# Kernel tuning notes

Measured on AMD Instinct MI355X. Metric: run time of the kernel, lower is better.

## Reference

```python
import jax, jax.numpy as jnp
import numpy as np

EPS = 1e-5  # GraphNorm eps


def setup_inputs() -> dict:
    key = jax.random.key(0)
    ks = jax.random.split(key, 8)
    B, N, D, L = 8, 2048, 128, 3
    return {
        "instance": jax.random.uniform(ks[0], (B, N, 2), jnp.float32),
        "Wn": jax.random.normal(ks[1], (D, 2), jnp.float32) * 0.5,
        "bn": jnp.zeros((D,), jnp.float32),
        "Wg": jax.random.normal(ks[2], (L, D, D), jnp.float32) / np.sqrt(D).astype(np.float32),
        "bg": jnp.zeros((L, D), jnp.float32),
        "gn_w": jnp.ones((D,), jnp.float32),
        "gn_b": jnp.zeros((D,), jnp.float32),
        "gn_a": jnp.ones((D,), jnp.float32),
    }


def reference(instance, Wn, bn, Wg, bg, gn_w, gn_b, gn_a):
    # instance: [B, N, 2] city coordinates. Graph is complete, so the PyG
    # edge-list GCN over all (i != j) pairs + self-loops is exactly a dense
    # symmetric-normalized adjacency matmul per graph.
    B, N, _ = instance.shape
    # pairwise Euclidean distances (cdist), safe sqrt to keep diagonal exact 0
    sq = jnp.sum(instance * instance, axis=-1)                      # [B, N]
    d2 = sq[:, :, None] + sq[:, None, :] - 2.0 * jnp.einsum(
        'bnd,bmd->bnm', instance, instance)                          # [B, N, N]
    pos = d2 > 0
    dist = jnp.where(pos, jnp.sqrt(jnp.where(pos, d2, 1.0)), 0.0)    # [B, N, N]
    # GCN edge weights = distances, self-loops added with weight 1.0
    A = dist + jnp.eye(N, dtype=dist.dtype)
    deg = jnp.sum(A, axis=-1)                                        # [B, N]
    dinv = jax.lax.rsqrt(deg)
    An = dinv[:, :, None] * A * dinv[:, None, :]                     # D^-1/2 A D^-1/2

    h = jnp.einsum('bne,de->bnd', instance, Wn) + bn                 # proj_node
    for l in range(Wg.shape[0]):
        # GCNConv: aggregate normalized messages of lin(x), then bias
        hw = jnp.einsum('bnm,bmd->bnd', An, jnp.einsum('bnd,ed->bne', h, Wg[l])) + bg[l]
        h = jnp.tanh(hw) + h                                         # activation + residual
        # GraphNorm (shared params across layers): per-graph, per-feature stats
        mean = jnp.mean(h, axis=1, keepdims=True)                    # [B, 1, D]
        sub = h - gn_a * mean
        var = jnp.mean(sub * sub, axis=1, keepdims=True)
        h = gn_w * sub * jax.lax.rsqrt(var + EPS) + gn_b
    return h  # [B, N, D] (unbatch+stack of equal-size graphs)
```

## Files before the change

kernel.cpp:

```cpp
#include <hip/hip_runtime.h>
#include <hip/hip_bf16.h>
#include <math.h>

#define BB 8
#define NN 2048
#define DD 128
#define LL 3
#define GN_EPS 1e-5f

typedef __attribute__((ext_vector_type(8))) short bf16x8;
typedef __attribute__((ext_vector_type(4))) float f32x4;
typedef __attribute__((ext_vector_type(8))) unsigned short u16x8;

#define FSQRT(x) __builtin_amdgcn_sqrtf(x)

__device__ __forceinline__ unsigned short f2bf(float f) {
    union { float f; unsigned u; } v; v.f = f;
    return (unsigned short)((v.u + 0x8000u) >> 16);
}

__device__ __forceinline__ float fast_tanh(float x) {
    float e = __expf(-2.0f * fabsf(x));
    float t = (1.0f - e) * __builtin_amdgcn_rcpf(1.0f + e);
    return copysignf(t, x);
}

__device__ __forceinline__ void stats_sc(float ps, float pq, float a, float w_,
                                         float b_, float& s, float& c) {
    const float inv_n = 1.0f / (float)NN;
    float mean = ps * inv_n;
    float msq  = pq * inv_n;
    float var  = msq - mean * mean * a * (2.0f - a);
    float rstd = rsqrtf(var + GN_EPS);
    s = w_ * rstd;
    c = b_ - s * (a * mean);
}


__global__ __launch_bounds__(256)
void prep_wg(const float* __restrict__ Wg, const float* __restrict__ Wn,
             const float* __restrict__ bn, unsigned short* __restrict__ wgf,
             float* __restrict__ weff, float* __restrict__ beff)
{
    const int f = blockIdx.x * 256 + threadIdx.x;
    const int l  = f >> 14;
    const int r  = f & 16383;
    const int dp = r >> 7;
    const int e  = r & 127;
    const int dpt = dp >> 4, ll = dp & 15;
    const int kc  = e >> 5,  eo = e & 31;
    wgf[((((l * 8 + dpt) * 4 + kc) * 16 + ll) << 5) + eo] = f2bf(Wg[f]);

    if (blockIdx.x == 0 && threadIdx.x < 128) {
        const int ee = threadIdx.x;
        float a0 = 0.f, a1 = 0.f, cc = 0.f;
        for (int d = 0; d < 128; ++d) {
            const float wv = Wg[ee * 128 + d];
            a0 = fmaf(wv, Wn[d * 2 + 0], a0);
            a1 = fmaf(wv, Wn[d * 2 + 1], a1);
            cc = fmaf(wv, bn[d], cc);
        }
        weff[ee * 2 + 0] = a0;
        weff[ee * 2 + 1] = a1;
        beff[ee] = cc;
    }
}

__global__ __launch_bounds__(256)
void gen_pack(const float* __restrict__ inst, const float* __restrict__ Wn,
              const float* __restrict__ bn, const float* __restrict__ weff,
              const float* __restrict__ beff,
              float* __restrict__ dinv, float* __restrict__ h,
              unsigned short* __restrict__ tp,
              float* __restrict__ psum, float* __restrict__ psq)
{
    __shared__ float cs[NN * 2];
    __shared__ float part[4][16];
    const int b     = blockIdx.x & 7;
    const int ntile = blockIdx.x >> 3;
    const int n0    = ntile * 16;
    const int tid   = threadIdx.x;
    const int w     = tid >> 6;
    const int lane  = tid & 63;
    const int lq    = lane >> 4;
    const int ll    = lane & 15;

    const float* instb = inst + b * NN * 2;
    for (int i = tid; i < (NN * 2) / 4; i += 256)
        ((float4*)cs)[i] = ((const float4*)instb)[i];
    __syncthreads();

    const int n = n0 + ll;
    const float nx = cs[n * 2 + 0];
    const float ny = cs[n * 2 + 1];

    const int diagkcg = ntile >> 1;
    float rs = 0.f;
    for (int kc = 0; kc < 16; ++kc) {
        const int kcg = w * 16 + kc;
        const int mb  = kcg * 32 + lq * 8;
        const float* cp = &cs[mb * 2];
        float4 c01 = *(const float4*)(cp + 0);
        float4 c23 = *(const float4*)(cp + 4);
        float4 c45 = *(const float4*)(cp + 8);
        float4 c67 = *(const float4*)(cp + 12);
        float mxx[8] = { c01.x, c01.z, c23.x, c23.z, c45.x, c45.z, c67.x, c67.z };
        float myy[8] = { c01.y, c01.w, c23.y, c23.w, c45.y, c45.w, c67.y, c67.w };
        float dist[8];
        #pragma unroll
        for (int j = 0; j < 8; ++j) {
            float dx = nx - mxx[j];
            float dy = ny - myy[j];
            dist[j] = FSQRT(dx * dx + dy * dy);
        }
        if (kcg == diagkcg) {
            #pragma unroll
            for (int j = 0; j < 8; ++j)
                if (mb + j == n) dist[j] = 1.0f;
        }
        #pragma unroll
        for (int j = 0; j < 8; ++j) rs += dist[j];
    }

    rs += __shfl_xor(rs, 16);
    rs += __shfl_xor(rs, 32);
    if (lq == 0) part[w][ll] = rs;
    __syncthreads();
    if (tid < 16)
        dinv[b * NN + n0 + tid] = rsqrtf(part[0][tid] + part[1][tid] +
                                         part[2][tid] + part[3][tid]);

    {
        const int d  = tid & 127;
        const int r0 = tid >> 7;
        const float w0 = Wn[d * 2 + 0];
        const float w1 = Wn[d * 2 + 1];
        const float bv = bn[d];
        const float we0 = weff[d * 2 + 0];
        const float we1 = weff[d * 2 + 1];
        const float be  = beff[d];
        const int kcg   = ntile >> 1;
        const int mbase = (ntile & 1) * 16;
        const int dt    = d >> 4;
        const int lld   = d & 15;
        unsigned short* tpd =
            tp + (((size_t)(b * 64 + kcg) * 8 + dt) * 64 + lld) * 8;
        #pragma unroll
        for (int r = r0; r < 16; r += 2) {
            const float x0 = cs[(n0 + r) * 2 + 0];
            const float x1 = cs[(n0 + r) * 2 + 1];
            h[((size_t)b * NN + n0 + r) * DD + d] = fmaf(x0, w0, fmaf(x1, w1, bv));
            const float dv = rsqrtf(part[0][r] + part[1][r] + part[2][r] + part[3][r]);
            const int mloc = mbase + r;
            const int lqa  = mloc >> 3;
            const int j    = mloc & 7;
            tpd[(size_t)lqa * 128 + j] = f2bf(dv * fmaf(x0, we0, fmaf(x1, we1, be)));
        }
    }
    if (blockIdx.x == 0) {
        for (int i = tid; i < LL * BB * DD; i += 256) { psum[i] = 0.f; psq[i] = 0.f; }
    }
}

template <bool HP>
__global__ __launch_bounds__(256)
void lin_mfma(const float* __restrict__ h, const unsigned short* __restrict__ wgf_l,
              const float* __restrict__ dinv,
              const float* __restrict__ psumP, const float* __restrict__ psqP,
              const float* __restrict__ ga, const float* __restrict__ gw,
              const float* __restrict__ gb, unsigned short* __restrict__ tp)
{
    __shared__ float sL[DD], cL[DD];
    const int tid  = threadIdx.x;
    const int b    = blockIdx.x & 7;
    const int tile = blockIdx.x >> 3;
    const int row0 = b * NN + tile * 32;
    const int w    = tid >> 6;
    const int lane = tid & 63;
    const int lq   = lane >> 4;
    const int ll   = lane & 15;

    if (tid < DD) {
        float s = 1.0f, c = 0.0f;
        if (HP)
            stats_sc(psumP[b * DD + tid], psqP[b * DD + tid],
                     ga[tid], gw[tid], gb[tid], s, c);
        sL[tid] = s; cL[tid] = c;
    }
    __syncthreads();

    bf16x8 aw[2][4];
    #pragma unroll
    for (int mt = 0; mt < 2; ++mt) {
        const int dpt = 2 * w + mt;
        #pragma unroll
        for (int kc = 0; kc < 4; ++kc)
            aw[mt][kc] = *(const bf16x8*)&wgf_l[(((dpt * 4 + kc) * 16 + ll) << 5) + lq * 8];
    }

    bf16x8 bh[2][4];
    #pragma unroll
    for (int nt = 0; nt < 2; ++nt) {
        const float* hrow = h + (size_t)(row0 + nt * 16 + ll) * DD;
        #pragma unroll
        for (int kc = 0; kc < 4; ++kc) {
            float4 h0 = *(const float4*)&hrow[kc * 32 + lq * 8];
            float4 h1 = *(const float4*)&hrow[kc * 32 + lq * 8 + 4];
            const int e0 = kc * 32 + lq * 8;
            bf16x8 p;
            p[0] = (short)f2bf(fmaf(sL[e0 + 0], h0.x, cL[e0 + 0]));
            p[1] = (short)f2bf(fmaf(sL[e0 + 1], h0.y, cL[e0 + 1]));
            p[2] = (short)f2bf(fmaf(sL[e0 + 2], h0.z, cL[e0 + 2]));
            p[3] = (short)f2bf(fmaf(sL[e0 + 3], h0.w, cL[e0 + 3]));
            p[4] = (short)f2bf(fmaf(sL[e0 + 4], h1.x, cL[e0 + 4]));
            p[5] = (short)f2bf(fmaf(sL[e0 + 5], h1.y, cL[e0 + 5]));
            p[6] = (short)f2bf(fmaf(sL[e0 + 6], h1.z, cL[e0 + 6]));
            p[7] = (short)f2bf(fmaf(sL[e0 + 7], h1.w, cL[e0 + 7]));
            bh[nt][kc] = p;
        }
    }

    f32x4 acc[2][2];
    #pragma unroll
    for (int i = 0; i < 2; ++i)
        #pragma unroll
        for (int j = 0; j < 2; ++j) acc[i][j] = (f32x4)0.0f;

    #pragma unroll
    for (int kc = 0; kc < 4; ++kc)
        #pragma unroll
        for (int nt = 0; nt < 2; ++nt)
            #pragma unroll
            for (int mt = 0; mt < 2; ++mt)
                acc[nt][mt] = __builtin_amdgcn_mfma_f32_16x16x32_bf16(
                    bh[nt][kc], aw[mt][kc], acc[nt][mt], 0, 0, 0);

    #pragma unroll
    for (int nt = 0; nt < 2; ++nt) {
        const int mloc0 = nt * 16 + lq * 4;
        const int lq_a  = mloc0 >> 3;
        const int j0    = mloc0 & 7;
        float4 di4 = *(const float4*)&dinv[row0 + mloc0];
        #pragma unroll
        for (int mt = 0; mt < 2; ++mt) {
            const int dt = 2 * w + mt;
            ushort4 pk;
            pk.x = f2bf(acc[nt][mt][0] * di4.x);
            pk.y = f2bf(acc[nt][mt][1] * di4.y);
            pk.z = f2bf(acc[nt][mt][2] * di4.z);
            pk.w = f2bf(acc[nt][mt][3] * di4.w);
            *(ushort4*)&tp[((size_t)((b * 64 + tile) * 8 + dt) * 64 + lq_a * 16 + ll) * 8 + j0] = pk;
        }
    }
}

template <bool HP>
__global__ __launch_bounds__(256, 2)
void agg_mfma(const float* __restrict__ inst, const unsigned short* __restrict__ tp,
              const float* __restrict__ dinv, const float* __restrict__ bg_l,
              const float* __restrict__ psumP, const float* __restrict__ psqP,
              const float* __restrict__ ga, const float* __restrict__ gw,
              const float* __restrict__ gb,
              float* __restrict__ h, float* __restrict__ psum, float* __restrict__ psq)
{
    __shared__ float cs[NN * 2];
    __shared__ char Abuf[64 * 1024];
    const int b    = blockIdx.x & 7;
    const int t2   = blockIdx.x >> 3;
    const int n0   = t2 * 32;
    const int tid  = threadIdx.x;
    const int w    = tid >> 6;
    const int lane = tid & 63;
    const int lq   = lane >> 4;
    const int ll   = lane & 15;

    const float* instb = inst + b * NN * 2;
    for (int i = tid; i < (NN * 2) / 4; i += 256)
        ((float4*)cs)[i] = ((const float4*)instb)[i];

    const unsigned short* tpb = tp + ((size_t)b * 64 * 8) * 512 + lane * 8;

    f32x4 acc[2][2];
    acc[0][0] = (f32x4)0.0f; acc[0][1] = (f32x4)0.0f;
    acc[1][0] = (f32x4)0.0f; acc[1][1] = (f32x4)0.0f;

    bf16x8 fbA0[4], fbA1[4], fbB0[4], fbB1[4];

    __syncthreads();

    const int   nr0 = n0 + ll;
    const int   nr1 = n0 + 16 + ll;
    const float nx0 = cs[nr0 * 2 + 0], ny0 = cs[nr0 * 2 + 1];
    const float nx1 = cs[nr1 * 2 + 0], ny1 = cs[nr1 * 2 + 1];

#define LOADB_INTO(B0, B1, KK) { \
        _Pragma("unroll") \
        for (int s_ = 0; s_ < 4; ++s_) { \
            B0[s_] = *(const bf16x8*)(tpb + (size_t)(((KK) * 4 + s_) * 8 + 2 * w + 0) * 512); \
            B1[s_] = *(const bf16x8*)(tpb + (size_t)(((KK) * 4 + s_) * 8 + 2 * w + 1) * 512); \
        } \
    }

#define GENPH(PH) { \
        _Pragma("unroll") \
        for (int q = 0; q < 8; ++q) { \
            const int kcg = (PH) * 32 + w * 8 + q; \
            const int mb  = kcg * 32 + lq * 8; \
            const float* cp = &cs[mb * 2]; \
            float4 c01 = *(const float4*)(cp + 0); \
            float4 c23 = *(const float4*)(cp + 4); \
            float4 c45 = *(const float4*)(cp + 8); \
            float4 c67 = *(const float4*)(cp + 12); \
            float mxx[8] = { c01.x, c01.z, c23.x, c23.z, c45.x, c45.z, c67.x, c67.z }; \
            float myy[8] = { c01.y, c01.w, c23.y, c23.w, c45.y, c45.w, c67.y, c67.w }; \
            const int slot0 = (2 * w + (q >> 2)) * 8 + (q & 3); \
            const bool dk = (kcg == t2); \
            u16x8 pk0, pk1; \
            _Pragma("unroll") \
            for (int j = 0; j < 8; ++j) { \
                float dx0 = nx0 - mxx[j], dy0 = ny0 - myy[j]; \
                float dv0 = FSQRT(dx0 * dx0 + dy0 * dy0); \
                if (dk && mb + j == nr0) dv0 = 1.0f; \
                pk0[j] = f2bf(dv0); \
                float dx1 = nx1 - mxx[j], dy1 = ny1 - myy[j]; \
                float dv1 = FSQRT(dx1 * dx1 + dy1 * dy1); \
                if (dk && mb + j == nr1) dv1 = 1.0f; \
                pk1[j] = f2bf(dv1); \
            } \
            *(u16x8*)(Abuf + (slot0 + 0) * 1024 + lane * 16) = pk0; \
            *(u16x8*)(Abuf + (slot0 + 4) * 1024 + lane * 16) = pk1; \
        } \
    }

#define STEP(I, C0, C1, DOLOAD, N0, N1, KN) { \
        bf16x8 af[2][4]; \
        _Pragma("unroll") \
        for (int nt = 0; nt < 2; ++nt) \
            _Pragma("unroll") \
            for (int s = 0; s < 4; ++s) \
                af[nt][s] = *(const bf16x8*)(Abuf + (((I) * 8 + nt * 4 + s) * 1024) + lane * 16); \
        if (DOLOAD) LOADB_INTO(N0, N1, KN) \
        _Pragma("unroll") \
        for (int s = 0; s < 4; ++s) \
            _Pragma("unroll") \
            for (int nt = 0; nt < 2; ++nt) { \
                acc[nt][0] = __builtin_amdgcn_mfma_f32_16x16x32_bf16(C0[s], af[nt][s], acc[nt][0], 0, 0, 0); \
                acc[nt][1] = __builtin_amdgcn_mfma_f32_16x16x32_bf16(C1[s], af[nt][s], acc[nt][1], 0, 0, 0); \
            } \
    }

    LOADB_INTO(fbA0, fbA1, 0)

    GENPH(0)
    __syncthreads();
    STEP(0, fbA0, fbA1, true,  fbB0, fbB1, 1)
    STEP(1, fbB0, fbB1, true,  fbA0, fbA1, 2)
    STEP(2, fbA0, fbA1, true,  fbB0, fbB1, 3)
    STEP(3, fbB0, fbB1, true,  fbA0, fbA1, 4)
    STEP(4, fbA0, fbA1, true,  fbB0, fbB1, 5)
    STEP(5, fbB0, fbB1, true,  fbA0, fbA1, 6)
    STEP(6, fbA0, fbA1, true,  fbB0, fbB1, 7)
    STEP(7, fbB0, fbB1, true,  fbA0, fbA1, 8)
    __syncthreads();

    GENPH(1)
    __syncthreads();
    STEP(0, fbA0, fbA1, true,  fbB0, fbB1, 9)
    STEP(1, fbB0, fbB1, true,  fbA0, fbA1, 10)
    STEP(2, fbA0, fbA1, true,  fbB0, fbB1, 11)
    STEP(3, fbB0, fbB1, true,  fbA0, fbA1, 12)
    STEP(4, fbA0, fbA1, true,  fbB0, fbB1, 13)
    STEP(5, fbB0, fbB1, true,  fbA0, fbA1, 14)
    STEP(6, fbA0, fbA1, true,  fbB0, fbB1, 15)
    STEP(7, fbB0, fbB1, false, fbA0, fbA1, 0)
    __syncthreads();

#undef STEP
#undef GENPH
#undef LOADB_INTO

    const float di0 = dinv[b * NN + n0 + ll];
    const float di1 = dinv[b * NN + n0 + 16 + ll];
    #pragma unroll
    for (int dtl = 0; dtl < 2; ++dtl) {
        const int d0 = (2 * w + dtl) * 16 + lq * 4;
        float4 bg4 = *(const float4*)&bg_l[d0];
        float sres[4] = {1.f, 1.f, 1.f, 1.f}, cres[4] = {0.f, 0.f, 0.f, 0.f};
        if (HP) {
            float4 ps4 = *(const float4*)&psumP[b * DD + d0];
            float4 pq4 = *(const float4*)&psqP[b * DD + d0];
            float4 ga4 = *(const float4*)&ga[d0];
            float4 gw4 = *(const float4*)&gw[d0];
            float4 gb4 = *(const float4*)&gb[d0];
            stats_sc(ps4.x, pq4.x, ga4.x, gw4.x, gb4.x, sres[0], cres[0]);
            stats_sc(ps4.y, pq4.y, ga4.y, gw4.y, gb4.y, sres[1], cres[1]);
            stats_sc(ps4.z, pq4.z, ga4.z, gw4.z, gb4.z, sres[2], cres[2]);
            stats_sc(ps4.w, pq4.w, ga4.w, gw4.w, gb4.w, sres[3], cres[3]);
        }
        float hs[4] = {0.f, 0.f, 0.f, 0.f}, hq[4] = {0.f, 0.f, 0.f, 0.f};
        #pragma unroll
        for (int nt = 0; nt < 2; ++nt) {
            const int n = n0 + nt * 16 + ll;
            const float di = nt ? di1 : di0;
            size_t idx = ((size_t)b * NN + n) * DD + d0;
            float4 hv = *(const float4*)&h[idx];
            float outv[4];
            #pragma unroll
            for (int r = 0; r < 4; ++r) {
                float pre = di * acc[nt][dtl][r] + (&bg4.x)[r];
                outv[r] = fast_tanh(pre) + fmaf(sres[r], (&hv.x)[r], cres[r]);
                hs[r] += outv[r];
                hq[r] += outv[r] * outv[r];
            }
            float4 ov = { outv[0], outv[1], outv[2], outv[3] };
            *(float4*)&h[idx] = ov;
        }

        #pragma unroll
        for (int off = 1; off < 16; off <<= 1) {
            #pragma unroll
            for (int r = 0; r < 4; ++r) {
                hs[r] += __shfl_xor(hs[r], off);
                hq[r] += __shfl_xor(hq[r], off);
            }
        }
        if (ll == 0) {
            #pragma unroll
            for (int r = 0; r < 4; ++r) {
                atomicAdd(&psum[b * DD + d0 + r], hs[r]);
                atomicAdd(&psq[b * DD + d0 + r], hq[r]);
            }
        }
    }
}

__global__ __launch_bounds__(256)
void apply_kernel(const float* __restrict__ h,
                  const float* __restrict__ psum2, const float* __restrict__ psq2,
                  const float* __restrict__ ga, const float* __restrict__ gw,
                  const float* __restrict__ gb, float* __restrict__ dst)
{
    const int i4 = blockIdx.x * 256 + threadIdx.x;
    const int dg = (i4 & 31) * 4;
    const int b  = i4 >> 16;
    float4 hv = ((const float4*)h)[i4];
    float o[4];
    #pragma unroll
    for (int j = 0; j < 4; ++j) {
        const int d = dg + j;
        float s, c;
        stats_sc(psum2[b * DD + d], psq2[b * DD + d], ga[d], gw[d], gb[d], s, c);
        o[j] = fmaf(s, (&hv.x)[j], c);
    }
    float4 ov = { o[0], o[1], o[2], o[3] };
    ((float4*)dst)[i4] = ov;
}

extern "C" void kernel_launch(void* const* d_in, const int* in_sizes, int n_in,
                              void* d_out, int out_size, void* d_ws, size_t ws_size,
                              hipStream_t stream)
{
    const float* inst = (const float*)d_in[0];
    const float* Wn   = (const float*)d_in[1];
    const float* bn   = (const float*)d_in[2];
    const float* Wg   = (const float*)d_in[3];
    const float* bg   = (const float*)d_in[4];
    const float* gw   = (const float*)d_in[5];
    const float* gb   = (const float*)d_in[6];
    const float* ga   = (const float*)d_in[7];
    float* out = (float*)d_out;

    float* ws   = (float*)d_ws;
    float* dinv = ws;
    float* h    = dinv + BB * NN;
    float* psum = h + (size_t)BB * NN * DD;
    float* psq  = psum + LL * BB * DD;
    float* weff = psq + LL * BB * DD;
    float* beff = weff + 2 * DD;
    unsigned short* wgf = (unsigned short*)(beff + DD);
    unsigned short* tp  = wgf + LL * DD * DD;

    prep_wg<<<(LL * DD * DD) / 256, 256, 0, stream>>>(Wg, Wn, bn, wgf, weff, beff);
    gen_pack<<<1024, 256, 0, stream>>>(inst, Wn, bn, weff, beff, dinv, h, tp, psum, psq);

    agg_mfma<false><<<512, 256, 0, stream>>>(
        inst, tp, dinv, bg + 0 * DD, nullptr, nullptr, ga, gw, gb, h, psum, psq);

    for (int l = 1; l < LL; ++l) {
        const unsigned short* wgl = wgf + (size_t)l * DD * DD;
        const float* psP = psum + (size_t)(l - 1) * BB * DD;
        const float* pqP = psq  + (size_t)(l - 1) * BB * DD;
        float* psL = psum + (size_t)l * BB * DD;
        float* pqL = psq  + (size_t)l * BB * DD;
        lin_mfma<true><<<(BB * NN) / 32, 256, 0, stream>>>(
            h, wgl, dinv, psP, pqP, ga, gw, gb, tp);
        agg_mfma<true><<<512, 256, 0, stream>>>(
            inst, tp, dinv, bg + l * DD, psP, pqP, ga, gw, gb, h, psL, pqL);
    }
    apply_kernel<<<(BB * NN * DD / 4) / 256, 256, 0, stream>>>(
        h, psum + 2 * BB * DD, psq + 2 * BB * DD, ga, gw, gb, out);
}
```

Baseline: 198.9 us.

## Double-buffer distance tiles in LDS and interleave generation with MFMA steps

Splits the 64KB adjacency staging buffer into two 32KB planes and generates the next quarter of on-the-fly distance tiles while MFMAs consume the current plane. Each wave now interleaves sqrt/bf16 packing with matrix instructions, so ALU and matrix work can overlap instead of running in separate phases. The number of block barriers grows, and register pressure goes up because generation temporaries are live alongside the B-fragment double buffers. The diagonal self-loop fix is hoisted under a per-tile branch.

```diff
diff --git a/kernel.cpp b/kernel.cpp
--- a/kernel.cpp
+++ b/kernel.cpp
@@ -264,7 +264,7 @@
               float* __restrict__ h, float* __restrict__ psum, float* __restrict__ psq)
 {
     __shared__ float cs[NN * 2];
-    __shared__ char Abuf[64 * 1024];
+    __shared__ __align__(16) char plane[2][32768];
     const int b    = blockIdx.x & 7;
     const int t2   = blockIdx.x >> 3;
     const int n0   = t2 * 32;
@@ -301,44 +301,45 @@
         } \
     }
 
-#define GENPH(PH) { \
+#define GENQ(PL, PH, Q) { \
+        const int kcg_ = (PH) * 16 + w * 4 + (Q); \
+        const int mb_  = kcg_ * 32 + lq * 8; \
+        const float* cp_ = &cs[mb_ * 2]; \
+        float4 c01 = *(const float4*)(cp_ + 0); \
+        float4 c23 = *(const float4*)(cp_ + 4); \
+        float4 c45 = *(const float4*)(cp_ + 8); \
+        float4 c67 = *(const float4*)(cp_ + 12); \
+        float mxx[8] = { c01.x, c01.z, c23.x, c23.z, c45.x, c45.z, c67.x, c67.z }; \
+        float myy[8] = { c01.y, c01.w, c23.y, c23.w, c45.y, c45.w, c67.y, c67.w }; \
+        float dv0[8], dv1[8]; \
         _Pragma("unroll") \
-        for (int q = 0; q < 8; ++q) { \
-            const int kcg = (PH) * 32 + w * 8 + q; \
-            const int mb  = kcg * 32 + lq * 8; \
-            const float* cp = &cs[mb * 2]; \
-            float4 c01 = *(const float4*)(cp + 0); \
-            float4 c23 = *(const float4*)(cp + 4); \
-            float4 c45 = *(const float4*)(cp + 8); \
-            float4 c67 = *(const float4*)(cp + 12); \
-            float mxx[8] = { c01.x, c01.z, c23.x, c23.z, c45.x, c45.z, c67.x, c67.z }; \
-            float myy[8] = { c01.y, c01.w, c23.y, c23.w, c45.y, c45.w, c67.y, c67.w }; \
-            const int slot0 = (2 * w + (q >> 2)) * 8 + (q & 3); \
-            const bool dk = (kcg == t2); \
-            u16x8 pk0, pk1; \
+        for (int j = 0; j < 8; ++j) { \
+            float dx0 = nx0 - mxx[j], dy0 = ny0 - myy[j]; \
+            dv0[j] = FSQRT(dx0 * dx0 + dy0 * dy0); \
+            float dx1 = nx1 - mxx[j], dy1 = ny1 - myy[j]; \
+            dv1[j] = FSQRT(dx1 * dx1 + dy1 * dy1); \
+        } \
+        if (kcg_ == t2) {    \
             _Pragma("unroll") \
             for (int j = 0; j < 8; ++j) { \
-                float dx0 = nx0 - mxx[j], dy0 = ny0 - myy[j]; \
-                float dv0 = FSQRT(dx0 * dx0 + dy0 * dy0); \
-                if (dk && mb + j == nr0) dv0 = 1.0f; \
-                pk0[j] = f2bf(dv0); \
-                float dx1 = nx1 - mxx[j], dy1 = ny1 - myy[j]; \
-                float dv1 = FSQRT(dx1 * dx1 + dy1 * dy1); \
-                if (dk && mb + j == nr1) dv1 = 1.0f; \
-                pk1[j] = f2bf(dv1); \
+                if (mb_ + j == nr0) dv0[j] = 1.0f; \
+                if (mb_ + j == nr1) dv1[j] = 1.0f; \
             } \
-            *(u16x8*)(Abuf + (slot0 + 0) * 1024 + lane * 16) = pk0; \
-            *(u16x8*)(Abuf + (slot0 + 4) * 1024 + lane * 16) = pk1; \
         } \
-    }
-
-#define STEP(I, C0, C1, DOLOAD, N0, N1, KN) { \
+        u16x8 pk0, pk1; \
+        _Pragma("unroll") \
+        for (int j = 0; j < 8; ++j) { pk0[j] = f2bf(dv0[j]); pk1[j] = f2bf(dv1[j]); } \
+        *(u16x8*)(plane[PL] + (w * 8 + 0 + (Q)) * 1024 + lane * 16) = pk0; \
+        *(u16x8*)(plane[PL] + (w * 8 + 4 + (Q)) * 1024 + lane * 16) = pk1; \
+    }
+
+#define STEP(PL, I, C0, C1, DOLOAD, N0, N1, KN) { \
         bf16x8 af[2][4]; \
         _Pragma("unroll") \
         for (int nt = 0; nt < 2; ++nt) \
             _Pragma("unroll") \
             for (int s = 0; s < 4; ++s) \
-                af[nt][s] = *(const bf16x8*)(Abuf + (((I) * 8 + nt * 4 + s) * 1024) + lane * 16); \
+                af[nt][s] = *(const bf16x8*)(plane[PL] + (((I) * 8 + nt * 4 + s) * 1024) + lane * 16); \
         if (DOLOAD) LOADB_INTO(N0, N1, KN) \
         _Pragma("unroll") \
         for (int s = 0; s < 4; ++s) \
@@ -349,34 +350,35 @@
             } \
     }
 
+    GENQ(0, 0, 0) GENQ(0, 0, 1) GENQ(0, 0, 2) GENQ(0, 0, 3)
     LOADB_INTO(fbA0, fbA1, 0)
-
-    GENPH(0)
-    __syncthreads();
-    STEP(0, fbA0, fbA1, true,  fbB0, fbB1, 1)
-    STEP(1, fbB0, fbB1, true,  fbA0, fbA1, 2)
-    STEP(2, fbA0, fbA1, true,  fbB0, fbB1, 3)
-    STEP(3, fbB0, fbB1, true,  fbA0, fbA1, 4)
-    STEP(4, fbA0, fbA1, true,  fbB0, fbB1, 5)
-    STEP(5, fbB0, fbB1, true,  fbA0, fbA1, 6)
-    STEP(6, fbA0, fbA1, true,  fbB0, fbB1, 7)
-    STEP(7, fbB0, fbB1, true,  fbA0, fbA1, 8)
-    __syncthreads();
-
-    GENPH(1)
-    __syncthreads();
-    STEP(0, fbA0, fbA1, true,  fbB0, fbB1, 9)
-    STEP(1, fbB0, fbB1, true,  fbA0, fbA1, 10)
-    STEP(2, fbA0, fbA1, true,  fbB0, fbB1, 11)
-    STEP(3, fbB0, fbB1, true,  fbA0, fbA1, 12)
-    STEP(4, fbA0, fbA1, true,  fbB0, fbB1, 13)
-    STEP(5, fbB0, fbB1, true,  fbA0, fbA1, 14)
-    STEP(6, fbA0, fbA1, true,  fbB0, fbB1, 15)
-    STEP(7, fbB0, fbB1, false, fbA0, fbA1, 0)
-    __syncthreads();
+    __syncthreads();
+
+    STEP(0, 0, fbA0, fbA1, true, fbB0, fbB1, 1)   GENQ(1, 1, 0)
+    STEP(0, 1, fbB0, fbB1, true, fbA0, fbA1, 2)   GENQ(1, 1, 1)
+    STEP(0, 2, fbA0, fbA1, true, fbB0, fbB1, 3)   GENQ(1, 1, 2)
+    STEP(0, 3, fbB0, fbB1, true, fbA0, fbA1, 4)   GENQ(1, 1, 3)
+    __syncthreads();
+
+    STEP(1, 0, fbA0, fbA1, true, fbB0, fbB1, 5)   GENQ(0, 2, 0)
+    STEP(1, 1, fbB0, fbB1, true, fbA0, fbA1, 6)   GENQ(0, 2, 1)
+    STEP(1, 2, fbA0, fbA1, true, fbB0, fbB1, 7)   GENQ(0, 2, 2)
+    STEP(1, 3, fbB0, fbB1, true, fbA0, fbA1, 8)   GENQ(0, 2, 3)
+    __syncthreads();
+
+    STEP(0, 0, fbA0, fbA1, true, fbB0, fbB1, 9)   GENQ(1, 3, 0)
+    STEP(0, 1, fbB0, fbB1, true, fbA0, fbA1, 10)  GENQ(1, 3, 1)
+    STEP(0, 2, fbA0, fbA1, true, fbB0, fbB1, 11)  GENQ(1, 3, 2)
+    STEP(0, 3, fbB0, fbB1, true, fbA0, fbA1, 12)  GENQ(1, 3, 3)
+    __syncthreads();
+
+    STEP(1, 0, fbA0, fbA1, true,  fbB0, fbB1, 13)
+    STEP(1, 1, fbB0, fbB1, true,  fbA0, fbA1, 14)
+    STEP(1, 2, fbA0, fbA1, true,  fbB0, fbB1, 15)
+    STEP(1, 3, fbB0, fbB1, false, fbA0, fbA1, 0)
 
 #undef STEP
-#undef GENPH
+#undef GENQ
 #undef LOADB_INTO
 
     const float di0 = dinv[b * NN + n0 + ll];
```

Result: faster. 176.4 us (-11.3%).
